# Kernel tuning notes

Hardware: AMD Instinct MI355X
Metric: run time of the kernel (lower is better)

The kernel has to match this reference:

```python
import jax, jax.numpy as jnp
import numpy as np

B, T, D, H = 4096, 512, 1, 64

def _uniform(k, shape, scale):
    return jax.random.uniform(k, shape, jnp.float32, -scale, scale)

def setup_inputs() -> dict:
    key = jax.random.key(0)
    ks = jax.random.split(key, 12)
    s = 1.0 / np.sqrt(H)  # torch nn.LSTM init scale
    return {
        "x": jax.random.normal(ks[0], (B, T, D), jnp.float32),
        # layer 0 (input_size=D)
        "W_ih0": _uniform(ks[1], (4 * H, D), s),
        "W_hh0": _uniform(ks[2], (4 * H, H), s),
        "b_ih0": _uniform(ks[3], (4 * H,), s),
        "b_hh0": _uniform(ks[4], (4 * H,), s),
        # layer 1 (input_size=H)
        "W_ih1": _uniform(ks[5], (4 * H, H), s),
        "W_hh1": _uniform(ks[6], (4 * H, H), s),
        "b_ih1": _uniform(ks[7], (4 * H,), s),
        "b_hh1": _uniform(ks[8], (4 * H,), s),
        # final projection to scalar
        "W_fc": _uniform(ks[9], (1, H), s),
        "b_fc": _uniform(ks[10], (1,), s),
    }

def _lstm_layer(x_seq, W_ih, W_hh, b_ih, b_hh):
    # x_seq: (B, T, Din) -> hidden sequence (B, T, H). Gate order: i, f, g, o.
    b, t, _ = x_seq.shape
    h = W_hh.shape[1]
    # precompute input contribution for all timesteps: (T, B, 4H)
    x_proj = jnp.einsum('btd,gd->tbg', x_seq, W_ih) + b_ih + b_hh
    Whh_T = W_hh.T  # (H, 4H)

    def step(carry, xp):
        h_t, c_t = carry
        gates = xp + h_t @ Whh_T  # (B, 4H)
        i_g, f_g, g_g, o_g = jnp.split(gates, 4, axis=-1)
        i_g = jax.nn.sigmoid(i_g)
        f_g = jax.nn.sigmoid(f_g)
        g_g = jnp.tanh(g_g)
        o_g = jax.nn.sigmoid(o_g)
        c_t = f_g * c_t + i_g * g_g
        h_t = o_g * jnp.tanh(c_t)
        return (h_t, c_t), h_t

    h0 = jnp.zeros((b, h), x_seq.dtype)
    (_, _), hs = jax.lax.scan(step, (h0, h0), x_proj)  # hs: (T, B, H)
    return jnp.swapaxes(hs, 0, 1)

def reference(x, W_ih0, W_hh0, b_ih0, b_hh0, W_ih1, W_hh1, b_ih1, b_hh1, W_fc, b_fc):
    h1 = _lstm_layer(x, W_ih0, W_hh0, b_ih0, b_hh0)   # (B, T, H)
    h2 = _lstm_layer(h1, W_ih1, W_hh1, b_ih1, b_hh1)  # (B, T, H)
    last = h2[:, -1, :]                                # (B, H)
    return last @ W_fc.T + b_fc                        # (B, 1)
```

## Files before the change

kernel.cpp:

```cpp
#include <hip/hip_runtime.h>


#define TT 512
#define HH 64
#define NB 16
#define XP 516

typedef __bf16 bf16_t;
typedef bf16_t bf16x8 __attribute__((ext_vector_type(8)));
typedef float  f32x4  __attribute__((ext_vector_type(4)));
typedef float  f32x2  __attribute__((ext_vector_type(2)));

#define MFMA(A, B, C) __builtin_amdgcn_mfma_f32_16x16x32_bf16((A), (B), (C), 0, 0, 0)
#define RCPF(x) __builtin_amdgcn_rcpf(x)

#if __has_builtin(__builtin_amdgcn_exp2f)
#define EXP2F(x) __builtin_amdgcn_exp2f(x)
#else
__device__ __forceinline__ float EXP2F(float x) {
    float r;
    asm volatile("v_exp_f32 %0, %1" : "=v"(r) : "v"(x));
    return r;
}
#endif

#define SC_IFO (-1.4426950408889634f)
#define SC_G   ( 2.8853900817779268f)

__device__ __forceinline__ unsigned short f32_to_bf16_rne(float f) {
    unsigned int u = __builtin_bit_cast(unsigned int, f);
    unsigned int r = u + 0x7fffu + ((u >> 16) & 1u);
    return (unsigned short)(r >> 16);
}
__device__ __forceinline__ float bf16bits_to_f32(unsigned short s) {
    return __builtin_bit_cast(float, ((unsigned int)s) << 16);
}
__device__ __forceinline__ bf16_t bits_to_bf16(unsigned short u) {
    return __builtin_bit_cast(bf16_t, u);
}
__device__ __forceinline__ void build_frags_scaled(const float* __restrict__ p, float sc,
                                                   bf16x8& hi, bf16x8& lo) {
    const float4 a = *(const float4*)p;
    const float4 b = *(const float4*)(p + 4);
    float v[8] = {a.x, a.y, a.z, a.w, b.x, b.y, b.z, b.w};
#pragma unroll
    for (int jj = 0; jj < 8; ++jj) {
        const float s = v[jj] * sc;
        unsigned short h = f32_to_bf16_rne(s);
        float d = s - bf16bits_to_f32(h);
        hi[jj] = bits_to_bf16(h);
        lo[jj] = bits_to_bf16(f32_to_bf16_rne(d));
    }
}

__device__ __forceinline__ f32x2 exp2v(f32x2 v) {
    f32x2 r; r[0] = EXP2F(v[0]); r[1] = EXP2F(v[1]); return r;
}
__device__ __forceinline__ f32x2 rcpv(f32x2 v) {
    f32x2 r; r[0] = RCPF(v[0]); r[1] = RCPF(v[1]); return r;
}
__device__ __forceinline__ f32x2 cell2(const f32x4 a0, const f32x4 a1, f32x2* c) {
    f32x2 is = {a0[0], a1[0]}, fs = {a0[1], a1[1]};
    f32x2 gs = {a0[2], a1[2]}, os = {a0[3], a1[3]};
    const f32x2 pf = exp2v(fs);
    const f32x2 fg = rcpv(1.0f + pf);
    const f32x2 pi = exp2v(is);
    const f32x2 e2 = exp2v(gs);
    const f32x2 z  = (e2 - 1.0f) * rcpv((1.0f + pi) * (1.0f + e2));
    *c = fg * (*c) + z;
    const f32x2 po  = exp2v(os);
    const f32x2 e2c = exp2v((*c) * SC_G);
    return (e2c - 1.0f) * rcpv((1.0f + po) * (1.0f + e2c));
}

__device__ __forceinline__ int imin2(int a, int b) { return a < b ? a : b; }

__global__ __launch_bounds__(768, 3)
void lstm_ff_kernel(const float* __restrict__ x,
                    const float* __restrict__ Wih0, const float* __restrict__ Whh0,
                    const float* __restrict__ bih0, const float* __restrict__ bhh0,
                    const float* __restrict__ Wih1, const float* __restrict__ Whh1,
                    const float* __restrict__ bih1, const float* __restrict__ bhh1,
                    const float* __restrict__ Wfc,  const float* __restrict__ bfc,
                    float* __restrict__ out)
{
    __shared__ float xbuf[NB][XP];
    __shared__ unsigned short h0r[8][NB][64];
    __shared__ unsigned short h1r[2][NB][64];
    __shared__ float h1fin[HH][NB + 1];
    __shared__ __align__(16) int f0[4];
    __shared__ __align__(16) int f1[8];

    const int tid  = threadIdx.x;
    const int wv   = tid >> 6;
    const int lane = tid & 63;
    const int m    = lane & 15;
    const int q    = lane >> 4;
    const int m7   = m & 7;
    const int b0   = blockIdx.x * NB;
    const bool isL0 = (wv < 4);

    for (int i = tid; i < NB * TT / 4; i += 768) {
        const int b  = i >> 7;
        const int t4 = i & 127;
        *(float4*)&xbuf[b][t4 * 4] = *(const float4*)&x[(size_t)(b0 + b) * TT + t4 * 4];
    }
    for (int i = tid; i < 8 * NB * 64; i += 768) (&h0r[0][0][0])[i] = 0;
    for (int i = tid; i < 2 * NB * 64; i += 768) (&h1r[0][0][0])[i] = 0;
    if (tid < 4) f0[tid] = -1;
    if (tid < 8) f1[tid] = -1;

    int roff[2];
#pragma unroll
    for (int kt = 0; kt < 2; ++kt)
        roff[kt] = m * 64 + (((4 * kt + q) ^ m7) * 8);

    const int gate_m = m & 3;
    const float scA  = (gate_m == 2) ? SC_G : SC_IFO;
    unsigned short* const H0 = &h0r[0][0][0];
    unsigned short* const H1 = &h1r[0][0][0];

    __syncthreads();

    if (isL0) {
        const int w = wv;
        bf16x8 Ah[4][2], Al[4][2];
        f32x4 bb0s[4], wx0s[4];
        int woff[4];
#pragma unroll
        for (int tau = 0; tau < 4; ++tau) {
            const int rowA = 64 * gate_m + 16 * w + 4 * tau + (m >> 2);
#pragma unroll
            for (int kt = 0; kt < 2; ++kt)
                build_frags_scaled(&Whh0[rowA * HH + kt * 32 + q * 8], scA,
                                   Ah[tau][kt], Al[tau][kt]);
#pragma unroll
            for (int r = 0; r < 4; ++r) {
                const int row = 64 * r + 16 * w + 4 * tau + q;
                const float sc = (r == 2) ? SC_G : SC_IFO;
                bb0s[tau][r] = (bih0[row] + bhh0[row]) * sc;
                wx0s[tau][r] = Wih0[row] * sc;
            }
            const int u = 16 * w + 4 * tau + q;
            woff[tau] = m * 64 + (((u >> 3) ^ m7) * 8) + (u & 7);
        }

        f32x2 cA = {0.f, 0.f}, cB = {0.f, 0.f};

#pragma unroll 1
        for (int t = 0; t < TT; ++t) {
            while (true) {
                const int4 v = *(const int4*)f0;
                if (imin2(imin2(v.x, v.y), imin2(v.z, v.w)) >= t - 1) break;
                asm volatile("" ::: "memory");
                __builtin_amdgcn_s_sleep(1);
            }
            asm volatile("" ::: "memory");

            const int rs = ((t - 1) & 7) * (NB * 64);
            bf16x8 h0[2];
            h0[0] = *(const bf16x8*)(H0 + rs + roff[0]);
            h0[1] = *(const bf16x8*)(H0 + rs + roff[1]);
            const float xv = xbuf[m][t];

            f32x4 a[4];
#pragma unroll
            for (int tau = 0; tau < 4; ++tau) {
                f32x4 p;
#pragma unroll
                for (int r = 0; r < 4; ++r)
                    p[r] = __builtin_fmaf(xv, wx0s[tau][r], bb0s[tau][r]);
                f32x4 z = {0.f, 0.f, 0.f, 0.f};
                p = MFMA(Ah[tau][0], h0[0], p);
                p = MFMA(Al[tau][0], h0[0], p);
                z = MFMA(Ah[tau][1], h0[1], z);
                z = MFMA(Al[tau][1], h0[1], z);
                a[tau] = p + z;
            }

            while (true) {
                const int4 va = *(const int4*)f1;
                const int4 vb = *(const int4*)(f1 + 4);
                const int mn = imin2(imin2(imin2(va.x, va.y), imin2(va.z, va.w)),
                                     imin2(imin2(vb.x, vb.y), imin2(vb.z, vb.w)));
                if (mn >= t - 8) break;
                asm volatile("" ::: "memory");
                __builtin_amdgcn_s_sleep(1);
            }
            asm volatile("" ::: "memory");

            const f32x2 hv0 = cell2(a[0], a[1], &cA);
            const f32x2 hv1 = cell2(a[2], a[3], &cB);

            const int ws = (t & 7) * (NB * 64);
            H0[ws + woff[0]] = f32_to_bf16_rne(hv0[0]);
            H0[ws + woff[1]] = f32_to_bf16_rne(hv0[1]);
            H0[ws + woff[2]] = f32_to_bf16_rne(hv1[0]);
            H0[ws + woff[3]] = f32_to_bf16_rne(hv1[1]);

            asm volatile("s_waitcnt lgkmcnt(0)" ::: "memory");
            if (lane == 0) *(volatile int*)&f0[w] = t;
        }
    } else {
        const int uW = wv - 4;
        bf16x8 Ah[2][4], Al[2][4];
        f32x4 bb1s[2];
        int woff[2], uu[2];
#pragma unroll
        for (int tau = 0; tau < 2; ++tau) {
            const int rowA = 64 * gate_m + 8 * uW + 4 * tau + (m >> 2);
#pragma unroll
            for (int kt = 0; kt < 2; ++kt)
                build_frags_scaled(&Wih1[rowA * HH + kt * 32 + q * 8], scA,
                                   Ah[tau][kt], Al[tau][kt]);
#pragma unroll
            for (int kt = 0; kt < 2; ++kt)
                build_frags_scaled(&Whh1[rowA * HH + kt * 32 + q * 8], scA,
                                   Ah[tau][2 + kt], Al[tau][2 + kt]);
#pragma unroll
            for (int r = 0; r < 4; ++r) {
                const int row = 64 * r + 8 * uW + 4 * tau + q;
                const float sc = (r == 2) ? SC_G : SC_IFO;
                bb1s[tau][r] = (bih1[row] + bhh1[row]) * sc;
            }
            const int u = 8 * uW + 4 * tau + q;
            uu[tau]   = u;
            woff[tau] = m * 64 + (((u >> 3) ^ m7) * 8) + (u & 7);
        }

        f32x2 c1 = {0.f, 0.f};

#pragma unroll 1
        for (int t = 0; t < TT; ++t) {
            while (true) {
                const int4 v = *(const int4*)f0;
                if (imin2(imin2(v.x, v.y), imin2(v.z, v.w)) >= t) break;
                asm volatile("" ::: "memory");
                __builtin_amdgcn_s_sleep(1);
            }
            asm volatile("" ::: "memory");
            const int rs0 = (t & 7) * (NB * 64);
            bf16x8 h0[2];
            h0[0] = *(const bf16x8*)(H0 + rs0 + roff[0]);
            h0[1] = *(const bf16x8*)(H0 + rs0 + roff[1]);

            while (true) {
                const int4 va = *(const int4*)f1;
                const int4 vb = *(const int4*)(f1 + 4);
                const int mn = imin2(imin2(imin2(va.x, va.y), imin2(va.z, va.w)),
                                     imin2(imin2(vb.x, vb.y), imin2(vb.z, vb.w)));
                if (mn >= t - 1) break;
                asm volatile("" ::: "memory");
                __builtin_amdgcn_s_sleep(1);
            }
            asm volatile("" ::: "memory");
            const int rs1 = ((t - 1) & 1) * (NB * 64);
            bf16x8 h1[2];
            h1[0] = *(const bf16x8*)(H1 + rs1 + roff[0]);
            h1[1] = *(const bf16x8*)(H1 + rs1 + roff[1]);

            f32x4 a[2];
#pragma unroll
            for (int tau = 0; tau < 2; ++tau) {
                f32x4 p = bb1s[tau];
                f32x4 s = {0.f, 0.f, 0.f, 0.f};
                p = MFMA(Ah[tau][0], h0[0], p);
                p = MFMA(Al[tau][0], h0[0], p);
                p = MFMA(Ah[tau][1], h0[1], p);
                p = MFMA(Al[tau][1], h0[1], p);
                s = MFMA(Ah[tau][2], h1[0], s);
                s = MFMA(Al[tau][2], h1[0], s);
                s = MFMA(Ah[tau][3], h1[1], s);
                s = MFMA(Al[tau][3], h1[1], s);
                a[tau] = p + s;
            }

            const f32x2 hv = cell2(a[0], a[1], &c1);
            if (t == TT - 1) {
                h1fin[uu[0]][m] = hv[0];
                h1fin[uu[1]][m] = hv[1];
            }
            const int ws = (t & 1) * (NB * 64);
            H1[ws + woff[0]] = f32_to_bf16_rne(hv[0]);
            H1[ws + woff[1]] = f32_to_bf16_rne(hv[1]);

            asm volatile("s_waitcnt lgkmcnt(0)" ::: "memory");
            if (lane == 0) *(volatile int*)&f1[uW] = t;
        }
    }

    __syncthreads();

    if (tid < NB) {
        float sacc = bfc[0];
#pragma unroll
        for (int u = 0; u < HH; ++u) sacc = fmaf(h1fin[u][tid], Wfc[u], sacc);
        out[b0 + tid] = sacc;
    }
}

extern "C" void kernel_launch(void* const* d_in, const int* in_sizes, int n_in,
                              void* d_out, int out_size, void* d_ws, size_t ws_size,
                              hipStream_t stream) {
    const float* x    = (const float*)d_in[0];
    const float* Wih0 = (const float*)d_in[1];
    const float* Whh0 = (const float*)d_in[2];
    const float* bih0 = (const float*)d_in[3];
    const float* bhh0 = (const float*)d_in[4];
    const float* Wih1 = (const float*)d_in[5];
    const float* Whh1 = (const float*)d_in[6];
    const float* bih1 = (const float*)d_in[7];
    const float* bhh1 = (const float*)d_in[8];
    const float* Wfc  = (const float*)d_in[9];
    const float* bfc  = (const float*)d_in[10];

    lstm_ff_kernel<<<dim3(4096 / NB), dim3(768), 0, stream>>>(
        x, Wih0, Whh0, bih0, bhh0, Wih1, Whh1, bih1, bhh1, Wfc, bfc, (float*)d_out);
}
```

Measured before the change: 518.7 us.

## Split layer-0 across eight waves and prefetch layer-1 recurrent term before waiting

Raises the block from 12 to 16 waves, so layer 0 uses 8 waves with half the gate tiles each, which shortens the per-step serial chain of the layer-0 recurrence. Layer 1 now computes its W_hh·h1 contribution first, while waiting for layer 0's output, then adds the W_ih·h0 term, overlapping the dependency wait with useful MFMA work. The costs are more waves competing for SIMD issue, an eight-entry flag poll for layer 0, and launch bounds that may limit registers or occupancy.

```diff
diff --git a/kernel.cpp b/kernel.cpp
--- a/kernel.cpp
+++ b/kernel.cpp
@@ -74,21 +74,27 @@
 }
 
 __device__ __forceinline__ int imin2(int a, int b) { return a < b ? a : b; }
-
-__global__ __launch_bounds__(768, 3)
-void lstm_ff_kernel(const float* __restrict__ x,
-                    const float* __restrict__ Wih0, const float* __restrict__ Whh0,
-                    const float* __restrict__ bih0, const float* __restrict__ bhh0,
-                    const float* __restrict__ Wih1, const float* __restrict__ Whh1,
-                    const float* __restrict__ bih1, const float* __restrict__ bhh1,
-                    const float* __restrict__ Wfc,  const float* __restrict__ bfc,
-                    float* __restrict__ out)
+__device__ __forceinline__ int min8(const int* f) {
+    const int4 a = *(const int4*)f;
+    const int4 b = *(const int4*)(f + 4);
+    return imin2(imin2(imin2(a.x, a.y), imin2(a.z, a.w)),
+                 imin2(imin2(b.x, b.y), imin2(b.z, b.w)));
+}
+
+__global__ __launch_bounds__(1024, 4)
+void lstm_ff16_kernel(const float* __restrict__ x,
+                      const float* __restrict__ Wih0, const float* __restrict__ Whh0,
+                      const float* __restrict__ bih0, const float* __restrict__ bhh0,
+                      const float* __restrict__ Wih1, const float* __restrict__ Whh1,
+                      const float* __restrict__ bih1, const float* __restrict__ bhh1,
+                      const float* __restrict__ Wfc,  const float* __restrict__ bfc,
+                      float* __restrict__ out)
 {
     __shared__ float xbuf[NB][XP];
     __shared__ unsigned short h0r[8][NB][64];
     __shared__ unsigned short h1r[2][NB][64];
     __shared__ float h1fin[HH][NB + 1];
-    __shared__ __align__(16) int f0[4];
+    __shared__ __align__(16) int f0[8];
     __shared__ __align__(16) int f1[8];
 
     const int tid  = threadIdx.x;
@@ -98,17 +104,17 @@
     const int q    = lane >> 4;
     const int m7   = m & 7;
     const int b0   = blockIdx.x * NB;
-    const bool isL0 = (wv < 4);
-
-    for (int i = tid; i < NB * TT / 4; i += 768) {
+    const bool isL0 = (wv < 8);
+
+    for (int i = tid; i < NB * TT / 4; i += 1024) {
         const int b  = i >> 7;
         const int t4 = i & 127;
         *(float4*)&xbuf[b][t4 * 4] = *(const float4*)&x[(size_t)(b0 + b) * TT + t4 * 4];
     }
-    for (int i = tid; i < 8 * NB * 64; i += 768) (&h0r[0][0][0])[i] = 0;
-    for (int i = tid; i < 2 * NB * 64; i += 768) (&h1r[0][0][0])[i] = 0;
-    if (tid < 4) f0[tid] = -1;
-    if (tid < 8) f1[tid] = -1;
+    for (int i = tid; i < 8 * NB * 64; i += 1024) (&h0r[0][0][0])[i] = 0;
+    for (int i = tid; i < 2 * NB * 64; i += 1024) (&h1r[0][0][0])[i] = 0;
+    if (tid < 8) f0[tid] = -1;
+    else if (tid < 16) f1[tid - 8] = -1;
 
     int roff[2];
 #pragma unroll
@@ -124,34 +130,33 @@
 
     if (isL0) {
         const int w = wv;
-        bf16x8 Ah[4][2], Al[4][2];
-        f32x4 bb0s[4], wx0s[4];
-        int woff[4];
-#pragma unroll
-        for (int tau = 0; tau < 4; ++tau) {
-            const int rowA = 64 * gate_m + 16 * w + 4 * tau + (m >> 2);
+        bf16x8 Ah[2][2], Al[2][2];
+        f32x4 bb0s[2], wx0s[2];
+        int woff[2];
+#pragma unroll
+        for (int tau = 0; tau < 2; ++tau) {
+            const int rowA = 64 * gate_m + 8 * w + 4 * tau + (m >> 2);
 #pragma unroll
             for (int kt = 0; kt < 2; ++kt)
                 build_frags_scaled(&Whh0[rowA * HH + kt * 32 + q * 8], scA,
                                    Ah[tau][kt], Al[tau][kt]);
 #pragma unroll
             for (int r = 0; r < 4; ++r) {
-                const int row = 64 * r + 16 * w + 4 * tau + q;
+                const int row = 64 * r + 8 * w + 4 * tau + q;
                 const float sc = (r == 2) ? SC_G : SC_IFO;
                 bb0s[tau][r] = (bih0[row] + bhh0[row]) * sc;
                 wx0s[tau][r] = Wih0[row] * sc;
             }
-            const int u = 16 * w + 4 * tau + q;
+            const int u = 8 * w + 4 * tau + q;
             woff[tau] = m * 64 + (((u >> 3) ^ m7) * 8) + (u & 7);
         }
 
-        f32x2 cA = {0.f, 0.f}, cB = {0.f, 0.f};
+        f32x2 cA = {0.f, 0.f};
 
 #pragma unroll 1
         for (int t = 0; t < TT; ++t) {
             while (true) {
-                const int4 v = *(const int4*)f0;
-                if (imin2(imin2(v.x, v.y), imin2(v.z, v.w)) >= t - 1) break;
+                if (min8(f0) >= t - 1) break;
                 asm volatile("" ::: "memory");
                 __builtin_amdgcn_s_sleep(1);
             }
@@ -163,9 +168,9 @@
             h0[1] = *(const bf16x8*)(H0 + rs + roff[1]);
             const float xv = xbuf[m][t];
 
-            f32x4 a[4];
-#pragma unroll
-            for (int tau = 0; tau < 4; ++tau) {
+            f32x4 a[2];
+#pragma unroll
+            for (int tau = 0; tau < 2; ++tau) {
                 f32x4 p;
 #pragma unroll
                 for (int r = 0; r < 4; ++r)
@@ -179,51 +184,44 @@
             }
 
             while (true) {
-                const int4 va = *(const int4*)f1;
-                const int4 vb = *(const int4*)(f1 + 4);
-                const int mn = imin2(imin2(imin2(va.x, va.y), imin2(va.z, va.w)),
-                                     imin2(imin2(vb.x, vb.y), imin2(vb.z, vb.w)));
-                if (mn >= t - 8) break;
+                if (min8(f1) >= t - 8) break;
                 asm volatile("" ::: "memory");
                 __builtin_amdgcn_s_sleep(1);
             }
             asm volatile("" ::: "memory");
 
-            const f32x2 hv0 = cell2(a[0], a[1], &cA);
-            const f32x2 hv1 = cell2(a[2], a[3], &cB);
-
+            const f32x2 hv = cell2(a[0], a[1], &cA);
             const int ws = (t & 7) * (NB * 64);
-            H0[ws + woff[0]] = f32_to_bf16_rne(hv0[0]);
-            H0[ws + woff[1]] = f32_to_bf16_rne(hv0[1]);
-            H0[ws + woff[2]] = f32_to_bf16_rne(hv1[0]);
-            H0[ws + woff[3]] = f32_to_bf16_rne(hv1[1]);
+            H0[ws + woff[0]] = f32_to_bf16_rne(hv[0]);
+            H0[ws + woff[1]] = f32_to_bf16_rne(hv[1]);
 
             asm volatile("s_waitcnt lgkmcnt(0)" ::: "memory");
             if (lane == 0) *(volatile int*)&f0[w] = t;
         }
     } else {
-        const int uW = wv - 4;
-        bf16x8 Ah[2][4], Al[2][4];
+        const int u1 = wv - 8;
+        bf16x8 Bih[2][2], Bil[2][2];
+        bf16x8 Bhh[2][2], Bhl[2][2];
         f32x4 bb1s[2];
         int woff[2], uu[2];
 #pragma unroll
         for (int tau = 0; tau < 2; ++tau) {
-            const int rowA = 64 * gate_m + 8 * uW + 4 * tau + (m >> 2);
+            const int rowA = 64 * gate_m + 8 * u1 + 4 * tau + (m >> 2);
 #pragma unroll
             for (int kt = 0; kt < 2; ++kt)
                 build_frags_scaled(&Wih1[rowA * HH + kt * 32 + q * 8], scA,
-                                   Ah[tau][kt], Al[tau][kt]);
+                                   Bih[tau][kt], Bil[tau][kt]);
 #pragma unroll
             for (int kt = 0; kt < 2; ++kt)
                 build_frags_scaled(&Whh1[rowA * HH + kt * 32 + q * 8], scA,
-                                   Ah[tau][2 + kt], Al[tau][2 + kt]);
+                                   Bhh[tau][kt], Bhl[tau][kt]);
 #pragma unroll
             for (int r = 0; r < 4; ++r) {
-                const int row = 64 * r + 8 * uW + 4 * tau + q;
+                const int row = 64 * r + 8 * u1 + 4 * tau + q;
                 const float sc = (r == 2) ? SC_G : SC_IFO;
                 bb1s[tau][r] = (bih1[row] + bhh1[row]) * sc;
             }
-            const int u = 8 * uW + 4 * tau + q;
+            const int u = 8 * u1 + 4 * tau + q;
             uu[tau]   = u;
             woff[tau] = m * 64 + (((u >> 3) ^ m7) * 8) + (u & 7);
         }
@@ -233,8 +231,29 @@
 #pragma unroll 1
         for (int t = 0; t < TT; ++t) {
             while (true) {
-                const int4 v = *(const int4*)f0;
-                if (imin2(imin2(v.x, v.y), imin2(v.z, v.w)) >= t) break;
+                if (min8(f1) >= t - 1) break;
+                asm volatile("" ::: "memory");
+                __builtin_amdgcn_s_sleep(1);
+            }
+            asm volatile("" ::: "memory");
+            const int rs1 = ((t - 1) & 1) * (NB * 64);
+            bf16x8 h1[2];
+            h1[0] = *(const bf16x8*)(H1 + rs1 + roff[0]);
+            h1[1] = *(const bf16x8*)(H1 + rs1 + roff[1]);
+
+            f32x4 s[2];
+#pragma unroll
+            for (int tau = 0; tau < 2; ++tau) {
+                f32x4 acc = bb1s[tau];
+                acc = MFMA(Bhh[tau][0], h1[0], acc);
+                acc = MFMA(Bhl[tau][0], h1[0], acc);
+                acc = MFMA(Bhh[tau][1], h1[1], acc);
+                acc = MFMA(Bhl[tau][1], h1[1], acc);
+                s[tau] = acc;
+            }
+
+            while (true) {
+                if (min8(f0) >= t) break;
                 asm volatile("" ::: "memory");
                 __builtin_amdgcn_s_sleep(1);
             }
@@ -244,35 +263,15 @@
             h0[0] = *(const bf16x8*)(H0 + rs0 + roff[0]);
             h0[1] = *(const bf16x8*)(H0 + rs0 + roff[1]);
 
-            while (true) {
-                const int4 va = *(const int4*)f1;
-                const int4 vb = *(const int4*)(f1 + 4);
-                const int mn = imin2(imin2(imin2(va.x, va.y), imin2(va.z, va.w)),
-                                     imin2(imin2(vb.x, vb.y), imin2(vb.z, vb.w)));
-                if (mn >= t - 1) break;
-                asm volatile("" ::: "memory");
-                __builtin_amdgcn_s_sleep(1);
-            }
-            asm volatile("" ::: "memory");
-            const int rs1 = ((t - 1) & 1) * (NB * 64);
-            bf16x8 h1[2];
-            h1[0] = *(const bf16x8*)(H1 + rs1 + roff[0]);
-            h1[1] = *(const bf16x8*)(H1 + rs1 + roff[1]);
-
             f32x4 a[2];
 #pragma unroll
             for (int tau = 0; tau < 2; ++tau) {
-                f32x4 p = bb1s[tau];
-                f32x4 s = {0.f, 0.f, 0.f, 0.f};
-                p = MFMA(Ah[tau][0], h0[0], p);
-                p = MFMA(Al[tau][0], h0[0], p);
-                p = MFMA(Ah[tau][1], h0[1], p);
-                p = MFMA(Al[tau][1], h0[1], p);
-                s = MFMA(Ah[tau][2], h1[0], s);
-                s = MFMA(Al[tau][2], h1[0], s);
-                s = MFMA(Ah[tau][3], h1[1], s);
-                s = MFMA(Al[tau][3], h1[1], s);
-                a[tau] = p + s;
+                f32x4 p = {0.f, 0.f, 0.f, 0.f};
+                p = MFMA(Bih[tau][0], h0[0], p);
+                p = MFMA(Bil[tau][0], h0[0], p);
+                p = MFMA(Bih[tau][1], h0[1], p);
+                p = MFMA(Bil[tau][1], h0[1], p);
+                a[tau] = p + s[tau];
             }
 
             const f32x2 hv = cell2(a[0], a[1], &c1);
@@ -285,7 +284,7 @@
             H1[ws + woff[1]] = f32_to_bf16_rne(hv[1]);
 
             asm volatile("s_waitcnt lgkmcnt(0)" ::: "memory");
-            if (lane == 0) *(volatile int*)&f1[uW] = t;
+            if (lane == 0) *(volatile int*)&f1[u1] = t;
         }
     }
 
@@ -314,6 +313,6 @@
     const float* Wfc  = (const float*)d_in[9];
     const float* bfc  = (const float*)d_in[10];
 
-    lstm_ff_kernel<<<dim3(4096 / NB), dim3(768), 0, stream>>>(
+    lstm_ff16_kernel<<<dim3(4096 / NB), dim3(1024), 0, stream>>>(
         x, Wih0, Whh0, bih0, bhh0, Wih1, Whh1, bih1, bhh1, Wfc, bfc, (float*)d_out);
 }
```

New measurement: 639.4 us. 23.3% more time.

## Deepen layer-0 ring to 32 slots and overlap layer-1 input projection with wait

Applied to the files above, without the earlier changes.

The layer-0 hidden-state ring buffer grows from 8 to 32 slots, and the layer-1 ring from 2 to 4. This lets layer-0 warps run further ahead of layer 1, and they now check the layer-1 progress flags only when their cached minimum falls out of range. Layer-1 warps compute the W_ih·h0 MFMAs before waiting on the layer-1 flags, so that input contribution overlaps the recurrent dependency wait, and they cache the layer-0 flag minimum to skip redundant polling. The cost is more shared memory (about 64KB for h0r), which may lower the number of resident blocks per CU below the declared three.

```diff
diff --git a/kernel.cpp b/kernel.cpp
--- a/kernel.cpp
+++ b/kernel.cpp
@@ -74,19 +74,29 @@
 }
 
 __device__ __forceinline__ int imin2(int a, int b) { return a < b ? a : b; }
+__device__ __forceinline__ int min4of(const int* f) {
+    const int4 v = *(const int4*)f;
+    return imin2(imin2(v.x, v.y), imin2(v.z, v.w));
+}
+__device__ __forceinline__ int min8of(const int* f) {
+    const int4 a = *(const int4*)f;
+    const int4 b = *(const int4*)(f + 4);
+    return imin2(imin2(imin2(a.x, a.y), imin2(a.z, a.w)),
+                 imin2(imin2(b.x, b.y), imin2(b.z, b.w)));
+}
 
 __global__ __launch_bounds__(768, 3)
-void lstm_ff_kernel(const float* __restrict__ x,
-                    const float* __restrict__ Wih0, const float* __restrict__ Whh0,
-                    const float* __restrict__ bih0, const float* __restrict__ bhh0,
-                    const float* __restrict__ Wih1, const float* __restrict__ Whh1,
-                    const float* __restrict__ bih1, const float* __restrict__ bhh1,
-                    const float* __restrict__ Wfc,  const float* __restrict__ bfc,
-                    float* __restrict__ out)
+void lstm_ff32_kernel(const float* __restrict__ x,
+                      const float* __restrict__ Wih0, const float* __restrict__ Whh0,
+                      const float* __restrict__ bih0, const float* __restrict__ bhh0,
+                      const float* __restrict__ Wih1, const float* __restrict__ Whh1,
+                      const float* __restrict__ bih1, const float* __restrict__ bhh1,
+                      const float* __restrict__ Wfc,  const float* __restrict__ bfc,
+                      float* __restrict__ out)
 {
     __shared__ float xbuf[NB][XP];
-    __shared__ unsigned short h0r[8][NB][64];
-    __shared__ unsigned short h1r[2][NB][64];
+    __shared__ unsigned short h0r[32][NB][64];
+    __shared__ unsigned short h1r[4][NB][64];
     __shared__ float h1fin[HH][NB + 1];
     __shared__ __align__(16) int f0[4];
     __shared__ __align__(16) int f1[8];
@@ -105,10 +115,10 @@
         const int t4 = i & 127;
         *(float4*)&xbuf[b][t4 * 4] = *(const float4*)&x[(size_t)(b0 + b) * TT + t4 * 4];
     }
-    for (int i = tid; i < 8 * NB * 64; i += 768) (&h0r[0][0][0])[i] = 0;
-    for (int i = tid; i < 2 * NB * 64; i += 768) (&h1r[0][0][0])[i] = 0;
+    for (int i = tid; i < 32 * NB * 64; i += 768) (&h0r[0][0][0])[i] = 0;
+    for (int i = tid; i < 4 * NB * 64; i += 768) (&h1r[0][0][0])[i] = 0;
     if (tid < 4) f0[tid] = -1;
-    if (tid < 8) f1[tid] = -1;
+    else if (tid < 12) f1[tid - 4] = -1;
 
     int roff[2];
 #pragma unroll
@@ -146,18 +156,26 @@
         }
 
         f32x2 cA = {0.f, 0.f}, cB = {0.f, 0.f};
+        int lastf1 = -1;
 
 #pragma unroll 1
         for (int t = 0; t < TT; ++t) {
-            while (true) {
-                const int4 v = *(const int4*)f0;
-                if (imin2(imin2(v.x, v.y), imin2(v.z, v.w)) >= t - 1) break;
+            while (min4of(f0) < t - 1) {
                 asm volatile("" ::: "memory");
                 __builtin_amdgcn_s_sleep(1);
             }
             asm volatile("" ::: "memory");
-
-            const int rs = ((t - 1) & 7) * (NB * 64);
+            if (lastf1 < t - 32) {
+                while (true) {
+                    lastf1 = min8of(f1);
+                    if (lastf1 >= t - 32) break;
+                    asm volatile("" ::: "memory");
+                    __builtin_amdgcn_s_sleep(1);
+                }
+                asm volatile("" ::: "memory");
+            }
+
+            const int rs = ((t - 1) & 31) * (NB * 64);
             bf16x8 h0[2];
             h0[0] = *(const bf16x8*)(H0 + rs + roff[0]);
             h0[1] = *(const bf16x8*)(H0 + rs + roff[1]);
@@ -178,21 +196,10 @@
                 a[tau] = p + z;
             }
 
-            while (true) {
-                const int4 va = *(const int4*)f1;
-                const int4 vb = *(const int4*)(f1 + 4);
-                const int mn = imin2(imin2(imin2(va.x, va.y), imin2(va.z, va.w)),
-                                     imin2(imin2(vb.x, vb.y), imin2(vb.z, vb.w)));
-                if (mn >= t - 8) break;
-                asm volatile("" ::: "memory");
-                __builtin_amdgcn_s_sleep(1);
-            }
-            asm volatile("" ::: "memory");
-
             const f32x2 hv0 = cell2(a[0], a[1], &cA);
             const f32x2 hv1 = cell2(a[2], a[3], &cB);
 
-            const int ws = (t & 7) * (NB * 64);
+            const int ws = (t & 31) * (NB * 64);
             H0[ws + woff[0]] = f32_to_bf16_rne(hv0[0]);
             H0[ws + woff[1]] = f32_to_bf16_rne(hv0[1]);
             H0[ws + woff[2]] = f32_to_bf16_rne(hv1[0]);
@@ -202,59 +209,69 @@
             if (lane == 0) *(volatile int*)&f0[w] = t;
         }
     } else {
-        const int uW = wv - 4;
-        bf16x8 Ah[2][4], Al[2][4];
+        const int u1 = wv - 4;
+        bf16x8 Bih[2][2], Bil[2][2];
+        bf16x8 Bhh[2][2], Bhl[2][2];
         f32x4 bb1s[2];
         int woff[2], uu[2];
 #pragma unroll
         for (int tau = 0; tau < 2; ++tau) {
-            const int rowA = 64 * gate_m + 8 * uW + 4 * tau + (m >> 2);
+            const int rowA = 64 * gate_m + 8 * u1 + 4 * tau + (m >> 2);
 #pragma unroll
             for (int kt = 0; kt < 2; ++kt)
                 build_frags_scaled(&Wih1[rowA * HH + kt * 32 + q * 8], scA,
-                                   Ah[tau][kt], Al[tau][kt]);
+                                   Bih[tau][kt], Bil[tau][kt]);
 #pragma unroll
             for (int kt = 0; kt < 2; ++kt)
                 build_frags_scaled(&Whh1[rowA * HH + kt * 32 + q * 8], scA,
-                                   Ah[tau][2 + kt], Al[tau][2 + kt]);
+                                   Bhh[tau][kt], Bhl[tau][kt]);
 #pragma unroll
             for (int r = 0; r < 4; ++r) {
-                const int row = 64 * r + 8 * uW + 4 * tau + q;
+                const int row = 64 * r + 8 * u1 + 4 * tau + q;
                 const float sc = (r == 2) ? SC_G : SC_IFO;
                 bb1s[tau][r] = (bih1[row] + bhh1[row]) * sc;
             }
-            const int u = 8 * uW + 4 * tau + q;
+            const int u = 8 * u1 + 4 * tau + q;
             uu[tau]   = u;
             woff[tau] = m * 64 + (((u >> 3) ^ m7) * 8) + (u & 7);
         }
 
         f32x2 c1 = {0.f, 0.f};
+        int lastf0 = -1;
 
 #pragma unroll 1
         for (int t = 0; t < TT; ++t) {
-            while (true) {
-                const int4 v = *(const int4*)f0;
-                if (imin2(imin2(v.x, v.y), imin2(v.z, v.w)) >= t) break;
+            if (lastf0 < t) {
+                while (true) {
+                    lastf0 = min4of(f0);
+                    if (lastf0 >= t) break;
+                    asm volatile("" ::: "memory");
+                    __builtin_amdgcn_s_sleep(1);
+                }
                 asm volatile("" ::: "memory");
-                __builtin_amdgcn_s_sleep(1);
-            }
-            asm volatile("" ::: "memory");
-            const int rs0 = (t & 7) * (NB * 64);
+            }
+            const int rs0 = (t & 31) * (NB * 64);
             bf16x8 h0[2];
             h0[0] = *(const bf16x8*)(H0 + rs0 + roff[0]);
             h0[1] = *(const bf16x8*)(H0 + rs0 + roff[1]);
 
-            while (true) {
-                const int4 va = *(const int4*)f1;
-                const int4 vb = *(const int4*)(f1 + 4);
-                const int mn = imin2(imin2(imin2(va.x, va.y), imin2(va.z, va.w)),
-                                     imin2(imin2(vb.x, vb.y), imin2(vb.z, vb.w)));
-                if (mn >= t - 1) break;
+            f32x4 p[2];
+#pragma unroll
+            for (int tau = 0; tau < 2; ++tau) {
+                f32x4 acc = bb1s[tau];
+                acc = MFMA(Bih[tau][0], h0[0], acc);
+                acc = MFMA(Bil[tau][0], h0[0], acc);
+                acc = MFMA(Bih[tau][1], h0[1], acc);
+                acc = MFMA(Bil[tau][1], h0[1], acc);
+                p[tau] = acc;
+            }
+
+            while (min8of(f1) < t - 1) {
                 asm volatile("" ::: "memory");
                 __builtin_amdgcn_s_sleep(1);
             }
             asm volatile("" ::: "memory");
-            const int rs1 = ((t - 1) & 1) * (NB * 64);
+            const int rs1 = ((t - 1) & 3) * (NB * 64);
             bf16x8 h1[2];
             h1[0] = *(const bf16x8*)(H1 + rs1 + roff[0]);
             h1[1] = *(const bf16x8*)(H1 + rs1 + roff[1]);
@@ -262,17 +279,12 @@
             f32x4 a[2];
 #pragma unroll
             for (int tau = 0; tau < 2; ++tau) {
-                f32x4 p = bb1s[tau];
                 f32x4 s = {0.f, 0.f, 0.f, 0.f};
-                p = MFMA(Ah[tau][0], h0[0], p);
-                p = MFMA(Al[tau][0], h0[0], p);
-                p = MFMA(Ah[tau][1], h0[1], p);
-                p = MFMA(Al[tau][1], h0[1], p);
-                s = MFMA(Ah[tau][2], h1[0], s);
-                s = MFMA(Al[tau][2], h1[0], s);
-                s = MFMA(Ah[tau][3], h1[1], s);
-                s = MFMA(Al[tau][3], h1[1], s);
-                a[tau] = p + s;
+                s = MFMA(Bhh[tau][0], h1[0], s);
+                s = MFMA(Bhl[tau][0], h1[0], s);
+                s = MFMA(Bhh[tau][1], h1[1], s);
+                s = MFMA(Bhl[tau][1], h1[1], s);
+                a[tau] = p[tau] + s;
             }
 
             const f32x2 hv = cell2(a[0], a[1], &c1);
@@ -280,12 +292,12 @@
                 h1fin[uu[0]][m] = hv[0];
                 h1fin[uu[1]][m] = hv[1];
             }
-            const int ws = (t & 1) * (NB * 64);
+            const int ws = (t & 3) * (NB * 64);
             H1[ws + woff[0]] = f32_to_bf16_rne(hv[0]);
             H1[ws + woff[1]] = f32_to_bf16_rne(hv[1]);
 
             asm volatile("s_waitcnt lgkmcnt(0)" ::: "memory");
-            if (lane == 0) *(volatile int*)&f1[uW] = t;
+            if (lane == 0) *(volatile int*)&f1[u1] = t;
         }
     }
 
@@ -314,6 +326,6 @@
     const float* Wfc  = (const float*)d_in[9];
     const float* bfc  = (const float*)d_in[10];
 
-    lstm_ff_kernel<<<dim3(4096 / NB), dim3(768), 0, stream>>>(
+    lstm_ff32_kernel<<<dim3(4096 / NB), dim3(768), 0, stream>>>(
         x, Wih0, Whh0, bih0, bhh0, Wih1, Whh1, bih1, bhh1, Wfc, bfc, (float*)d_out);
 }
```

Result: slower. 536.7 us (+3.5%).
